# Performance work log

Measured on AMD Instinct MI355X. Metric: run time of the kernel, lower is better.

The kernel has to match this reference:

```python
import jax, jax.numpy as jnp
import numpy as np

TEMPERATURE = 8.0  # sqrt(d_k) with d_k = 64
NEG_INF = -1e30    # finite stand-in for -inf; exp() underflows to 0 identically


def _skew(s):
    # Music-Transformer relative-position skew: F.pad(s,(1,0)).view(-1,L+1,L)[:,1:,:]
    B, L, _ = s.shape
    s = jnp.pad(s, ((0, 0), (0, 0), (1, 0)))  # [B, L, L+1]
    return s.reshape(B, L + 1, L)[:, 1:, :]   # [B, L, L]


def setup_inputs() -> dict:
    key = jax.random.key(0)
    kq, kk, kv, ke = jax.random.split(key, 4)
    B, L, D = 16, 2048, 64
    q = jax.random.normal(kq, (B, L, D), dtype=jnp.float32)
    k = jax.random.normal(kk, (B, L, D), dtype=jnp.float32)
    v = jax.random.normal(kv, (B, L, D), dtype=jnp.float32)
    e = jax.random.normal(ke, (B, L, D), dtype=jnp.float32)
    # causal mask (True = masked out), broadcast to batch
    mask = jnp.broadcast_to(jnp.triu(jnp.ones((L, L), dtype=bool), k=1), (B, L, L))
    return {"q": q, "k": k, "v": v, "e": e, "mask": mask}


def reference(q, k, v, e, mask):
    attn = jnp.einsum('bqd,bkd->bqk', q, k)          # q @ k^T
    attn = attn + _skew(jnp.einsum('bqd,bkd->bqk', q, e))
    attn = attn / TEMPERATURE
    attn = jnp.where(mask, NEG_INF, attn)
    attn = jax.nn.softmax(attn, axis=2)
    attn = jnp.where(mask, 0.0, attn)
    # dropout is identity in eval mode
    output = jnp.einsum('bqk,bkd->bqd', attn, v)
    return (output, attn)
```

## Files before the change

### kernel.cpp

```cpp
#include <hip/hip_runtime.h>

typedef unsigned int u32;
typedef __fp16 h2 __attribute__((ext_vector_type(2)));
typedef _Float16 f16x8 __attribute__((ext_vector_type(8)));
typedef float f32x4 __attribute__((ext_vector_type(4)));

#define BB 16
#define LL 2048
#define DD 64
#define RPB 16
#define NTHREADS 256
#define NBLK (LL / RPB)
#define NWG (BB * NBLK)
#define NXCD 8

__device__ __forceinline__ h2 pk(float x, float y) {
#if __has_builtin(__builtin_amdgcn_cvt_pkrtz)
    return __builtin_amdgcn_cvt_pkrtz(x, y);
#else
    h2 r; r.x = (__fp16)x; r.y = (__fp16)y; return r;
#endif
}

union F8U { f16x8 v; h2 p[4]; };
__device__ __forceinline__ f16x8 pack8(float4 a, float4 b) {
    F8U u;
    u.p[0] = pk(a.x, a.y); u.p[1] = pk(a.z, a.w);
    u.p[2] = pk(b.x, b.y); u.p[3] = pk(b.z, b.w);
    return u.v;
}
__device__ __forceinline__ f16x8 pack8s(const float* s) {
    F8U u;
    u.p[0] = pk(s[0], s[1]); u.p[1] = pk(s[2], s[3]);
    u.p[2] = pk(s[4], s[5]); u.p[3] = pk(s[6], s[7]);
    return u.v;
}

#define MFMA(A, B, C) __builtin_amdgcn_mfma_f32_16x16x32_f16((A), (B), (C), 0, 0, 0)

__device__ __forceinline__ void score_quad(
    int t, int wave, int o4, int lc, int r0,
    const float* __restrict__ kb, const float* __restrict__ eb,
    f16x8 qa0, f16x8 qa1, float s[4])
{
    const int c0w = (t << 6) + (wave << 4);

    const float* kr = kb + (size_t)(c0w + lc) * DD + 8 * o4;
    float4 k0 = *(const float4*)(kr);
    float4 k1 = *(const float4*)(kr + 4);
    float4 k2 = *(const float4*)(kr + 32);
    float4 k3 = *(const float4*)(kr + 36);

    const int j0w = c0w + 2032 - r0;
    int er0 = j0w + lc;      if (er0 > LL - 1) er0 = LL - 1;
    int er1 = j0w + 16 + lc; if (er1 > LL - 1) er1 = LL - 1;
    const float* e0p = eb + (size_t)er0 * DD + 8 * o4;
    const float* e1p = eb + (size_t)er1 * DD + 8 * o4;
    float4 ea0 = *(const float4*)(e0p);
    float4 ea1 = *(const float4*)(e0p + 4);
    float4 ea2 = *(const float4*)(e0p + 32);
    float4 ea3 = *(const float4*)(e0p + 36);
    float4 eb0 = *(const float4*)(e1p);
    float4 eb1 = *(const float4*)(e1p + 4);
    float4 eb2 = *(const float4*)(e1p + 32);
    float4 eb3 = *(const float4*)(e1p + 36);

    f16x8 kf0 = pack8(k0, k1), kf1 = pack8(k2, k3);
    f16x8 ef00 = pack8(ea0, ea1), ef01 = pack8(ea2, ea3);
    f16x8 ef10 = pack8(eb0, eb1), ef11 = pack8(eb2, eb3);

    const f32x4 z = {0.f, 0.f, 0.f, 0.f};
    f32x4 dk = MFMA(qa0, kf0, z);  dk = MFMA(qa1, kf1, dk);
    f32x4 g0 = MFMA(qa0, ef00, z); g0 = MFMA(qa1, ef01, g0);
    f32x4 g1 = MFMA(qa0, ef10, z); g1 = MFMA(qa1, ef11, g1);

#pragma unroll
    for (int i = 0; i < 4; ++i) {
        const int rl  = 4 * o4 + i;
        const int lj  = lc + 15 - rl;
        const int src = (o4 << 4) | (lj & 15);
        float ga = __shfl(g0[i], src, 64);
        float gb = __shfl(g1[i], src, 64);
        float gv = (lj < 16) ? ga : gb;
        float sv = (dk[i] + gv) * 0.125f;
        if (c0w + lc > r0 + rl) sv = -60000.f;
        s[i] = sv;
    }
}

__global__ __launch_bounds__(NTHREADS, 6) void attn_fused(
    const float* __restrict__ qg, const float* __restrict__ kg,
    const float* __restrict__ vg, const float* __restrict__ eg,
    float* __restrict__ out_o, float* __restrict__ out_attn)
{
    __shared__ __align__(16) __fp16 St[4][2][16][24];
    __shared__ float Ored[3][16][68];
    __shared__ float mred[16][4], lred[16][4], mfin[16], linvs[16];

    const int tid  = threadIdx.x;
    const int wave = tid >> 6;
    const int lane = tid & 63;
    const int o4   = lane >> 4;
    const int lc   = lane & 15;

    const int work = (blockIdx.x & (NXCD - 1)) * (NWG / NXCD) + (blockIdx.x >> 3);
    const int b    = work / NBLK;
    const int r0   = (NBLK - 1 - (work % NBLK)) * RPB;
    const size_t bLL = (size_t)b * LL;

    const float* qb = qg + bLL * DD;
    const float* kb = kg + bLL * DD;
    const float* eb = eg + bLL * DD;
    const float* vb = vg + bLL * DD;

    {
        const int z0 = r0 + RPB;
        const int nq = (LL - z0) >> 2;
        const float4 z4 = make_float4(0.f, 0.f, 0.f, 0.f);
        for (int ri = 0; ri < RPB; ++ri) {
            float4* zp = (float4*)(out_attn + (bLL + r0 + ri) * LL + z0);
            for (int i = tid; i < nq; i += NTHREADS) zp[i] = z4;
        }
    }

    f16x8 qa0, qa1;
    {
        const float* qr = qb + (size_t)(r0 + lc) * DD + 8 * o4;
        float4 a0 = *(const float4*)(qr);
        float4 a1 = *(const float4*)(qr + 4);
        float4 b0 = *(const float4*)(qr + 32);
        float4 b1 = *(const float4*)(qr + 36);
        qa0 = pack8(a0, a1);
        qa1 = pack8(b0, b1);
    }

    const int span = r0 + 15 - (wave << 4);
    const int nTw  = (span >= 0) ? ((span >> 6) + 1) : 0;

    float mrun[4] = {-60000.f, -60000.f, -60000.f, -60000.f};
    float lrun[4] = {0.f, 0.f, 0.f, 0.f};

    for (int t = 0; t < nTw; ++t) {
        float s[4];
        score_quad(t, wave, o4, lc, r0, kb, eb, qa0, qa1, s);
#pragma unroll
        for (int i = 0; i < 4; ++i) {
            float tm = s[i];
            tm = fmaxf(tm, __shfl_xor(tm, 1, 64));
            tm = fmaxf(tm, __shfl_xor(tm, 2, 64));
            tm = fmaxf(tm, __shfl_xor(tm, 4, 64));
            tm = fmaxf(tm, __shfl_xor(tm, 8, 64));
            float mn = fmaxf(mrun[i], tm);
            float sc = __expf(mrun[i] - mn);
            lrun[i] = lrun[i] * sc + __expf(s[i] - mn);
            mrun[i] = mn;
        }
    }
#pragma unroll
    for (int i = 0; i < 4; ++i) {
        float lt = lrun[i];
        lt += __shfl_xor(lt, 1, 64);
        lt += __shfl_xor(lt, 2, 64);
        lt += __shfl_xor(lt, 4, 64);
        lt += __shfl_xor(lt, 8, 64);
        if (lc == 0) { mred[4 * o4 + i][wave] = mrun[i]; lred[4 * o4 + i][wave] = lt; }
    }
    __syncthreads();
    if (tid < RPB) {
        float m = -60000.f;
#pragma unroll
        for (int w = 0; w < 4; ++w) m = fmaxf(m, mred[tid][w]);
        float l = 0.f;
#pragma unroll
        for (int w = 0; w < 4; ++w) l += lred[tid][w] * __expf(mred[tid][w] - m);
        mfin[tid]  = m;
        linvs[tid] = 1.f / l;
    }
    __syncthreads();

    float mF[4], iF[4];
#pragma unroll
    for (int i = 0; i < 4; ++i) { mF[i] = mfin[4 * o4 + i]; iF[i] = linvs[4 * o4 + i]; }

    f32x4 oacc[4];
#pragma unroll
    for (int dc = 0; dc < 4; ++dc) oacc[dc] = (f32x4){0.f, 0.f, 0.f, 0.f};

#define PV_PAIR(CE, CO) do {                                                       \
        f16x8 pa = *(const f16x8*)&St[wave][o4 >> 1][lc][(o4 & 1) << 3];           \
        const int vbase = (((o4) < 2) ? (CE) : (CO)) + ((o4 & 1) << 3);            \
        _Pragma("unroll")                                                          \
        for (int dc = 0; dc < 4; ++dc) {                                           \
            const float* vp = vb + (size_t)vbase * DD + dc * 16 + lc;              \
            float ve[8];                                                           \
            _Pragma("unroll")                                                      \
            for (int e = 0; e < 8; ++e) ve[e] = vp[(size_t)e * DD];                \
            f16x8 vf = pack8s(ve);                                                 \
            oacc[dc] = MFMA(pa, vf, oacc[dc]);                                     \
        }                                                                          \
    } while (0)

    for (int t = 0; t < nTw; ++t) {
        float s[4];
        score_quad(t, wave, o4, lc, r0, kb, eb, qa0, qa1, s);
        const int c = (t << 6) + (wave << 4) + lc;
        float p[4];
#pragma unroll
        for (int i = 0; i < 4; ++i) {
            p[i] = __expf(s[i] - mF[i]) * iF[i];
            out_attn[(bLL + r0 + 4 * o4 + i) * LL + c] = p[i];
            St[wave][t & 1][4 * o4 + i][lc] = (__fp16)p[i];
        }
        if (t & 1) {
            const int ce = ((t - 1) << 6) + (wave << 4);
            const int co = (t << 6) + (wave << 4);
            PV_PAIR(ce, co);
        }
    }
    if (nTw & 1) {
#pragma unroll
        for (int i = 0; i < 4; ++i) St[wave][1][4 * o4 + i][lc] = (__fp16)0.f;
        const int ce = ((nTw - 1) << 6) + (wave << 4);
        PV_PAIR(ce, ce);
    }

    if (wave > 0) {
#pragma unroll
        for (int dc = 0; dc < 4; ++dc)
#pragma unroll
            for (int i = 0; i < 4; ++i)
                Ored[wave - 1][4 * o4 + i][dc * 16 + lc] = oacc[dc][i];
    }
    __syncthreads();
    if (wave == 0) {
#pragma unroll
        for (int dc = 0; dc < 4; ++dc)
#pragma unroll
            for (int i = 0; i < 4; ++i) {
                const int rl = 4 * o4 + i, d = dc * 16 + lc;
                float o = oacc[dc][i] + Ored[0][rl][d] + Ored[1][rl][d] + Ored[2][rl][d];
                out_o[(bLL + r0 + rl) * DD + d] = o;
            }
    }
}

extern "C" void kernel_launch(void* const* d_in, const int* in_sizes, int n_in,
                              void* d_out, int out_size, void* d_ws, size_t ws_size,
                              hipStream_t stream) {
    const float* q = (const float*)d_in[0];
    const float* k = (const float*)d_in[1];
    const float* v = (const float*)d_in[2];
    const float* e = (const float*)d_in[3];
    float* out_o    = (float*)d_out;
    float* out_attn = out_o + (size_t)BB * LL * DD;

    dim3 grid(NWG);
    attn_fused<<<grid, NTHREADS, 0, stream>>>(q, k, v, e, out_o, out_attn);
}
```

Baseline: 812.4 us.

## Give each wave its own 16-row block with balanced causal pairing

```diff
diff --git a/kernel.cpp b/kernel.cpp
--- a/kernel.cpp
+++ b/kernel.cpp
@@ -8,10 +8,11 @@
 #define BB 16
 #define LL 2048
 #define DD 64
-#define RPB 16
+#define RPW 16
 #define NTHREADS 256
-#define NBLK (LL / RPB)
-#define NWG (BB * NBLK)
+#define RBB (LL / RPW)
+#define JPB (RBB / 4)
+#define NWG (BB * JPB)
 #define NXCD 8
 
 __device__ __forceinline__ h2 pk(float x, float y) {
@@ -39,12 +40,10 @@
 #define MFMA(A, B, C) __builtin_amdgcn_mfma_f32_16x16x32_f16((A), (B), (C), 0, 0, 0)
 
 __device__ __forceinline__ void score_quad(
-    int t, int wave, int o4, int lc, int r0,
+    int c0w, int o4, int lc, int r0,
     const float* __restrict__ kb, const float* __restrict__ eb,
     f16x8 qa0, f16x8 qa1, float s[4])
 {
-    const int c0w = (t << 6) + (wave << 4);
-
     const float* kr = kb + (size_t)(c0w + lc) * DD + 8 * o4;
     float4 k0 = *(const float4*)(kr);
     float4 k1 = *(const float4*)(kr + 4);
@@ -88,14 +87,12 @@
     }
 }
 
-__global__ __launch_bounds__(NTHREADS, 6) void attn_fused(
+__global__ __launch_bounds__(NTHREADS, 2) void attn_fused(
     const float* __restrict__ qg, const float* __restrict__ kg,
     const float* __restrict__ vg, const float* __restrict__ eg,
     float* __restrict__ out_o, float* __restrict__ out_attn)
 {
-    __shared__ __align__(16) __fp16 St[4][2][16][24];
-    __shared__ float Ored[3][16][68];
-    __shared__ float mred[16][4], lred[16][4], mfin[16], linvs[16];
+    __shared__ __align__(16) __fp16 St[4][16][72];
 
     const int tid  = threadIdx.x;
     const int wave = tid >> 6;
@@ -103,25 +100,19 @@
     const int o4   = lane >> 4;
     const int lc   = lane & 15;
 
-    const int work = (blockIdx.x & (NXCD - 1)) * (NWG / NXCD) + (blockIdx.x >> 3);
-    const int b    = work / NBLK;
-    const int r0   = (NBLK - 1 - (work % NBLK)) * RPB;
+    const int swz = (blockIdx.x & (NXCD - 1)) * (NWG / NXCD) + (blockIdx.x >> 3);
+    const int b   = swz / JPB;
+    const int j   = swz % JPB;
+    const int rb  = ((wave & 1) ? (2 * JPB - 1 - j) : j) + (wave >> 1) * (2 * JPB);
+    const int r0  = rb * RPW;
+    const int nT  = (rb >> 2) + 1;
+    const int nstL = (rb & 3) + 1;
     const size_t bLL = (size_t)b * LL;
 
     const float* qb = qg + bLL * DD;
     const float* kb = kg + bLL * DD;
     const float* eb = eg + bLL * DD;
     const float* vb = vg + bLL * DD;
-
-    {
-        const int z0 = r0 + RPB;
-        const int nq = (LL - z0) >> 2;
-        const float4 z4 = make_float4(0.f, 0.f, 0.f, 0.f);
-        for (int ri = 0; ri < RPB; ++ri) {
-            float4* zp = (float4*)(out_attn + (bLL + r0 + ri) * LL + z0);
-            for (int i = tid; i < nq; i += NTHREADS) zp[i] = z4;
-        }
-    }
 
     f16x8 qa0, qa1;
     {
@@ -134,114 +125,106 @@
         qa1 = pack8(b0, b1);
     }
 
-    const int span = r0 + 15 - (wave << 4);
-    const int nTw  = (span >= 0) ? ((span >> 6) + 1) : 0;
-
-    float mrun[4] = {-60000.f, -60000.f, -60000.f, -60000.f};
-    float lrun[4] = {0.f, 0.f, 0.f, 0.f};
-
-    for (int t = 0; t < nTw; ++t) {
-        float s[4];
-        score_quad(t, wave, o4, lc, r0, kb, eb, qa0, qa1, s);
-#pragma unroll
-        for (int i = 0; i < 4; ++i) {
-            float tm = s[i];
-            tm = fmaxf(tm, __shfl_xor(tm, 1, 64));
-            tm = fmaxf(tm, __shfl_xor(tm, 2, 64));
-            tm = fmaxf(tm, __shfl_xor(tm, 4, 64));
-            tm = fmaxf(tm, __shfl_xor(tm, 8, 64));
-            float mn = fmaxf(mrun[i], tm);
-            float sc = __expf(mrun[i] - mn);
-            lrun[i] = lrun[i] * sc + __expf(s[i] - mn);
-            mrun[i] = mn;
-        }
-    }
+    {
+        const int z0 = r0 + RPW;
+        const int nq = (LL - z0) >> 2;
+        const float4 z4 = make_float4(0.f, 0.f, 0.f, 0.f);
+        for (int ri = 0; ri < RPW; ++ri) {
+            float4* zp = (float4*)(out_attn + (bLL + r0 + ri) * LL + z0);
+            for (int i2 = lane; i2 < nq; i2 += 64) zp[i2] = z4;
+        }
+    }
+
+    float m[4] = {-60000.f, -60000.f, -60000.f, -60000.f};
+    float l[4] = {0.f, 0.f, 0.f, 0.f};
+
+    for (int t = 0; t < nT; ++t) {
+        const int nst = (t == nT - 1) ? nstL : 4;
+#pragma unroll
+        for (int st = 0; st < 4; ++st) {
+            if (st < nst) {
+                float s[4];
+                score_quad((t << 6) + (st << 4), o4, lc, r0, kb, eb, qa0, qa1, s);
+#pragma unroll
+                for (int i = 0; i < 4; ++i) {
+                    float mn = fmaxf(m[i], s[i]);
+                    l[i] = l[i] * __expf(m[i] - mn) + __expf(s[i] - mn);
+                    m[i] = mn;
+                }
+            }
+        }
+    }
+
+    float mF[4], iF[4];
 #pragma unroll
     for (int i = 0; i < 4; ++i) {
-        float lt = lrun[i];
-        lt += __shfl_xor(lt, 1, 64);
-        lt += __shfl_xor(lt, 2, 64);
-        lt += __shfl_xor(lt, 4, 64);
-        lt += __shfl_xor(lt, 8, 64);
-        if (lc == 0) { mred[4 * o4 + i][wave] = mrun[i]; lred[4 * o4 + i][wave] = lt; }
-    }
-    __syncthreads();
-    if (tid < RPB) {
-        float m = -60000.f;
-#pragma unroll
-        for (int w = 0; w < 4; ++w) m = fmaxf(m, mred[tid][w]);
-        float l = 0.f;
-#pragma unroll
-        for (int w = 0; w < 4; ++w) l += lred[tid][w] * __expf(mred[tid][w] - m);
-        mfin[tid]  = m;
-        linvs[tid] = 1.f / l;
-    }
-    __syncthreads();
-
-    float mF[4], iF[4];
-#pragma unroll
-    for (int i = 0; i < 4; ++i) { mF[i] = mfin[4 * o4 + i]; iF[i] = linvs[4 * o4 + i]; }
+        float mr = m[i];
+        mr = fmaxf(mr, __shfl_xor(mr, 1, 64));
+        mr = fmaxf(mr, __shfl_xor(mr, 2, 64));
+        mr = fmaxf(mr, __shfl_xor(mr, 4, 64));
+        mr = fmaxf(mr, __shfl_xor(mr, 8, 64));
+        float lr = l[i] * __expf(m[i] - mr);
+        lr += __shfl_xor(lr, 1, 64);
+        lr += __shfl_xor(lr, 2, 64);
+        lr += __shfl_xor(lr, 4, 64);
+        lr += __shfl_xor(lr, 8, 64);
+        mF[i] = mr;
+        iF[i] = 1.f / lr;
+    }
 
     f32x4 oacc[4];
 #pragma unroll
     for (int dc = 0; dc < 4; ++dc) oacc[dc] = (f32x4){0.f, 0.f, 0.f, 0.f};
 
-#define PV_PAIR(CE, CO) do {                                                       \
-        f16x8 pa = *(const f16x8*)&St[wave][o4 >> 1][lc][(o4 & 1) << 3];           \
-        const int vbase = (((o4) < 2) ? (CE) : (CO)) + ((o4 & 1) << 3);            \
-        _Pragma("unroll")                                                          \
-        for (int dc = 0; dc < 4; ++dc) {                                           \
-            const float* vp = vb + (size_t)vbase * DD + dc * 16 + lc;              \
-            float ve[8];                                                           \
-            _Pragma("unroll")                                                      \
-            for (int e = 0; e < 8; ++e) ve[e] = vp[(size_t)e * DD];                \
-            f16x8 vf = pack8s(ve);                                                 \
-            oacc[dc] = MFMA(pa, vf, oacc[dc]);                                     \
-        }                                                                          \
-    } while (0)
-
-    for (int t = 0; t < nTw; ++t) {
-        float s[4];
-        score_quad(t, wave, o4, lc, r0, kb, eb, qa0, qa1, s);
-        const int c = (t << 6) + (wave << 4) + lc;
-        float p[4];
-#pragma unroll
-        for (int i = 0; i < 4; ++i) {
-            p[i] = __expf(s[i] - mF[i]) * iF[i];
-            out_attn[(bLL + r0 + 4 * o4 + i) * LL + c] = p[i];
-            St[wave][t & 1][4 * o4 + i][lc] = (__fp16)p[i];
-        }
-        if (t & 1) {
-            const int ce = ((t - 1) << 6) + (wave << 4);
-            const int co = (t << 6) + (wave << 4);
-            PV_PAIR(ce, co);
-        }
-    }
-    if (nTw & 1) {
-#pragma unroll
-        for (int i = 0; i < 4; ++i) St[wave][1][4 * o4 + i][lc] = (__fp16)0.f;
-        const int ce = ((nTw - 1) << 6) + (wave << 4);
-        PV_PAIR(ce, ce);
-    }
-
-    if (wave > 0) {
-#pragma unroll
-        for (int dc = 0; dc < 4; ++dc)
-#pragma unroll
-            for (int i = 0; i < 4; ++i)
-                Ored[wave - 1][4 * o4 + i][dc * 16 + lc] = oacc[dc][i];
-    }
-    __syncthreads();
-    if (wave == 0) {
-#pragma unroll
-        for (int dc = 0; dc < 4; ++dc)
-#pragma unroll
-            for (int i = 0; i < 4; ++i) {
-                const int rl = 4 * o4 + i, d = dc * 16 + lc;
-                float o = oacc[dc][i] + Ored[0][rl][d] + Ored[1][rl][d] + Ored[2][rl][d];
-                out_o[(bLL + r0 + rl) * DD + d] = o;
+    for (int t = 0; t < nT; ++t) {
+        const int nst = (t == nT - 1) ? nstL : 4;
+        const int cb  = t << 6;
+
+        f16x8 vf[2][4];
+#pragma unroll
+        for (int kc = 0; kc < 2; ++kc) {
+#pragma unroll
+            for (int dc = 0; dc < 4; ++dc) {
+                const float* vp = vb + (size_t)(cb + (kc << 5) + (o4 << 3)) * DD + (dc << 4) + lc;
+                float ve[8];
+#pragma unroll
+                for (int e = 0; e < 8; ++e) ve[e] = vp[(size_t)e * DD];
+                vf[kc][dc] = pack8s(ve);
             }
-    }
+        }
+
+#pragma unroll
+        for (int st = 0; st < 4; ++st) {
+            if (st < nst) {
+                float s[4];
+                score_quad(cb + (st << 4), o4, lc, r0, kb, eb, qa0, qa1, s);
+#pragma unroll
+                for (int i = 0; i < 4; ++i) {
+                    float p = __expf(s[i] - mF[i]) * iF[i];
+                    out_attn[(bLL + r0 + 4 * o4 + i) * LL + cb + (st << 4) + lc] = p;
+                    St[wave][4 * o4 + i][(st << 4) + lc] = (__fp16)p;
+                }
+            } else {
+#pragma unroll
+                for (int i = 0; i < 4; ++i)
+                    St[wave][4 * o4 + i][(st << 4) + lc] = (__fp16)0.f;
+            }
+        }
+
+#pragma unroll
+        for (int kc = 0; kc < 2; ++kc) {
+            f16x8 pa = *(const f16x8*)&St[wave][lc][(kc << 5) + (o4 << 3)];
+#pragma unroll
+            for (int dc = 0; dc < 4; ++dc)
+                oacc[dc] = MFMA(pa, vf[kc][dc], oacc[dc]);
+        }
+    }
+
+#pragma unroll
+    for (int dc = 0; dc < 4; ++dc)
+#pragma unroll
+        for (int i = 0; i < 4; ++i)
+            out_o[(bLL + r0 + 4 * o4 + i) * DD + (dc << 4) + lc] = oacc[dc][i];
 }
 
 extern "C" void kernel_launch(void* const* d_in, const int* in_sizes, int n_in,
```

After: 881.7 us. +8.5%, slower.
